# Kernel tuning notes

Hardware: AMD Instinct MI355X
Metric: run time of the kernel (lower is better)

Reference implementation:

```python
import jax, jax.numpy as jnp
import numpy as np


def setup_inputs() -> dict:
    key = jax.random.key(0)
    ks = jax.random.split(key, 7)
    b, t, c = 2, 2048, 1024
    s = 0.02  # keep pre-softmax logits in a sane range
    return {
        "query": jax.random.normal(ks[0], (b, t, c), jnp.float32),
        "key": jax.random.normal(ks[1], (b, t, c), jnp.float32),
        "value": jax.random.normal(ks[2], (b, t, c), jnp.float32),
        "in_proj_w": jax.random.normal(ks[3], (3 * c, c), jnp.float32) * s,
        "in_proj_b": jax.random.normal(ks[4], (3 * c,), jnp.float32) * s,
        "out_proj_w": jax.random.normal(ks[5], (c, c), jnp.float32) * s,
        "out_proj_b": jax.random.normal(ks[6], (c,), jnp.float32) * s,
        "window_size": 128,
    }


def reference(query, key, value, in_proj_w, in_proj_b, out_proj_w, out_proj_b, window_size):
    num_heads = 16
    b, t, c = query.shape
    hd = c // num_heads
    wq, wk, wv = in_proj_w[:c], in_proj_w[c:2 * c], in_proj_w[2 * c:]
    bq, bk, bv = in_proj_b[:c], in_proj_b[c:2 * c], in_proj_b[2 * c:]
    # project and split heads: [b, h, t, hd]
    q = (query @ wq.T + bq).reshape(b, t, num_heads, hd).transpose(0, 2, 1, 3)
    k = (key @ wk.T + bk).reshape(b, t, num_heads, hd).transpose(0, 2, 1, 3)
    v = (value @ wv.T + bv).reshape(b, t, num_heads, hd).transpose(0, 2, 1, 3)
    # NOTE: torch adds a *float* attn_mask to the logits. The original mask is
    # 1.0 inside the sliding window, 0.0 outside -- an additive +1 bias, NOT -inf.
    idx = jnp.arange(t)
    band = (jnp.abs(idx[:, None] - idx[None, :]) <= window_size).astype(q.dtype)  # [t, t]
    scale = 1.0 / jnp.sqrt(jnp.asarray(hd, q.dtype))
    logits = jnp.einsum("bhqd,bhkd->bhqk", q * scale, k) + band  # [b,h,t,t]
    attn = jax.nn.softmax(logits, axis=-1)
    out = jnp.einsum("bhqk,bhkd->bhqd", attn, v)  # [b,h,t,hd]
    out = out.transpose(0, 2, 1, 3).reshape(b, t, c)
    return out @ out_proj_w.T + out_proj_b
```

## Files before the change

kernel.cpp:

```cpp
#include <hip/hip_runtime.h>

typedef __attribute__((ext_vector_type(8)))  short short8;
typedef __attribute__((ext_vector_type(4)))  float f32x4;
typedef __attribute__((ext_vector_type(16))) float f32x16;
typedef __attribute__((ext_vector_type(2)))  unsigned uint2v;

constexpr int B  = 2;
constexpr int T  = 2048;
constexpr int C  = 1024;
constexpr int H  = 16;
constexpr int HD = 64;

__device__ inline unsigned bf16rne(float a){
  unsigned u = __builtin_bit_cast(unsigned, a);
  u += 0x7fffu + ((u >> 16) & 1u);
  return u >> 16;
}
__device__ inline unsigned bf16pair(float a, float b){
  unsigned ua = __builtin_bit_cast(unsigned, a); ua += 0x7fffu + ((ua >> 16) & 1u);
  unsigned ub = __builtin_bit_cast(unsigned, b); ub += 0x7fffu + ((ub >> 16) & 1u);
  return (ua >> 16) | (ub & 0xffff0000u);
}
__device__ inline void gll16(const void* g, void* l){
  __builtin_amdgcn_global_load_lds(
      (const __attribute__((address_space(1))) unsigned*)g,
      (__attribute__((address_space(3))) unsigned*)l, 16, 0, 0);
}
__device__ inline float exp2f_(float x){
#if __has_builtin(__builtin_amdgcn_exp2f)
  return __builtin_amdgcn_exp2f(x);
#else
  return __builtin_exp2f(x);
#endif
}

__global__ void convert_k(const float* __restrict__ ipw, const float* __restrict__ opw,
                          const float* __restrict__ q, const float* __restrict__ k,
                          const float* __restrict__ v, unsigned* __restrict__ dst)
{
  const int i = blockIdx.x * 256 + threadIdx.x;
  const long e = (long)i * 8;
  const float* src; long off;
  if      (e <  3145728) { src = ipw; off = e; }
  else if (e <  4194304) { src = opw; off = e - 3145728; }
  else if (e <  8388608) { src = q;   off = e - 4194304; }
  else if (e < 12582912) { src = k;   off = e - 8388608; }
  else                   { src = v;   off = e - 12582912; }
  const float4 x0 = *(const float4*)(src + off);
  const float4 x1 = *(const float4*)(src + off + 4);
  uint4 st;
  st.x = bf16pair(x0.x, x0.y); st.y = bf16pair(x0.z, x0.w);
  st.z = bf16pair(x1.x, x1.y); st.w = bf16pair(x1.z, x1.w);
  *(uint4*)(dst + (size_t)i*4) = st;
}

__global__ __launch_bounds__(256, 3) void gemm_qkv(
    const unsigned short* __restrict__ A0, const unsigned short* __restrict__ A1,
    const unsigned short* __restrict__ A2,
    const unsigned short* __restrict__ Wb, const float* __restrict__ bias,
    unsigned short* __restrict__ Qb, unsigned short* __restrict__ Kf,
    unsigned short* __restrict__ Vf)
{
  __shared__ __align__(16) char gsm[32768];
  unsigned short* As = (unsigned short*)gsm;
  unsigned short* Bs = (unsigned short*)(gsm + 16384);

  const int tid  = threadIdx.x, lane = tid & 63, wv = tid >> 6;
  const int wm   = wv & 1, wn = wv >> 1;
  const int bm   = blockIdx.x, bn = blockIdx.y;
  const int m16  = lane & 15, quad = lane >> 4;

  const int which = bn >> 3;
  const unsigned short* A = (which == 0) ? A0 : (which == 1 ? A1 : A2);

  f32x4 acc[4][4];
#pragma unroll
  for (int i = 0; i < 4; i++)
#pragma unroll
    for (int j = 0; j < 4; j++) acc[i][j] = (f32x4){0.f, 0.f, 0.f, 0.f};

  const int srow = wv * 32 + (lane >> 3);
  const int skp  = (((lane & 7) ^ (lane >> 3))) * 8;
  const int xr   = m16 & 7;

  for (int k0 = 0; k0 < 1024; k0 += 64) {
    __syncthreads();
#pragma unroll
    for (int p = 0; p < 4; p++) {
      gll16(A  + (size_t)(bm*128 + srow + p*8)*1024 + k0 + skp, (char*)As + wv*4096 + p*1024);
      gll16(Wb + (size_t)(bn*128 + srow + p*8)*1024 + k0 + skp, (char*)Bs + wv*4096 + p*1024);
    }
    __syncthreads();

#pragma unroll
    for (int kk = 0; kk < 2; kk++) {
      const int ch = ((kk*4 + quad) ^ xr) * 16;
      short8 af[4], bf[4];
#pragma unroll
      for (int i = 0; i < 4; i++)
        af[i] = *(const short8*)((const char*)As + (wm*64 + i*16 + m16)*128 + ch);
#pragma unroll
      for (int j = 0; j < 4; j++)
        bf[j] = *(const short8*)((const char*)Bs + (wn*64 + j*16 + m16)*128 + ch);
#pragma unroll
      for (int i = 0; i < 4; i++)
#pragma unroll
        for (int j = 0; j < 4; j++)
          acc[i][j] = __builtin_amdgcn_mfma_f32_16x16x32_bf16(af[i], bf[j], acc[i][j], 0,0,0);
    }
  }

  __syncthreads();
  float* Ls = (float*)gsm;
  const int hbase = (bn & 7) * 2;
  const int b = bm >> 4;
  const int tbase = (bm & 15) * 128;
  const float ksc = (which == 1) ? 0.18033688f : 1.0f;

  if (which < 2) {
#pragma unroll
    for (int j = 0; j < 4; ++j) {
      const float bj = bias[bn*128 + wn*64 + j*16 + m16] * ksc;
#pragma unroll
      for (int i = 0; i < 4; ++i) {
        const int m0 = wm*64 + i*16 + quad*4;
#pragma unroll
        for (int r = 0; r < 4; ++r)
          Ls[(m0 + r)*36 + wn*16 + m16] = __builtin_fmaf(acc[i][j][r], ksc, bj);
      }
      __syncthreads();
#pragma unroll
      for (int r2 = 0; r2 < 2; ++r2) {
        const int v = r2*256 + tid;
        const int m = v & 127, seg = v >> 7;
        const int wn2 = seg >> 1;
        const float* src = &Ls[m*36 + wn2*16 + (seg & 1)*8];
        const float4 f0 = *(const float4*)src;
        const float4 f1 = *(const float4*)(src + 4);
        uint4 st;
        st.x = bf16pair(f0.x, f0.y); st.y = bf16pair(f0.z, f0.w);
        st.z = bf16pair(f1.x, f1.y); st.w = bf16pair(f1.z, f1.w);
        const int bhh = b*16 + hbase + wn2;
        if (which == 0) {
          const int d0 = j*16 + (seg & 1)*8;
          *(uint4*)&Qb[((size_t)(bhh*2048) + tbase + m)*64 + d0] = st;
        } else {
          const int kt = (tbase + m) >> 6;
          const int wkk = (m >> 5) & 1, ln2 = m & 31;
          const int h2 = seg & 1;
          uint4* dp = (uint4*)Kf + ((size_t)(bhh*32 + kt)*8 + j*2 + wkk)*64 + h2*32 + ln2;
          *dp = st;
        }
      }
      __syncthreads();
    }
  } else {
#pragma unroll
    for (int j = 0; j < 4; ++j) {
      const float bj = bias[bn*128 + wn*64 + j*16 + m16];
      const int col = wn*16 + m16;
#pragma unroll
      for (int i = 0; i < 4; ++i) {
        f32x4 tv = acc[i][j];
        tv[0] += bj; tv[1] += bj; tv[2] += bj; tv[3] += bj;
        *(f32x4*)&Ls[col*132 + wm*64 + i*16 + quad*4] = tv;
      }
      __syncthreads();
#pragma unroll
      for (int r2 = 0; r2 < 2; ++r2) {
        const int v = r2*256 + tid;
        const int n = v >> 4, mseg = v & 15;
        const float* src = &Ls[n*132 + mseg*8];
        const float4 f0 = *(const float4*)src;
        const float4 f1 = *(const float4*)(src + 4);
        uint4 st;
        st.x = bf16pair(f0.x, f0.y); st.y = bf16pair(f0.z, f0.w);
        st.z = bf16pair(f1.x, f1.y); st.w = bf16pair(f1.z, f1.w);
        const int d = j*16 + (n & 15);
        const int bhh = b*16 + hbase + (n >> 4);
        const int t0 = tbase + mseg*8;
        const int kt = t0 >> 6, tc = (t0 & 63) >> 3;
        const int wkk = tc >> 2, cc = (tc >> 1) & 1, h2 = tc & 1;
        const int dt = d >> 5, ln2 = d & 31;
        uint4* dp = (uint4*)Vf + (size_t)(bhh*32 + kt)*512 + dt*256 + cc*128 + wkk*64 + h2*32 + ln2;
        *dp = st;
      }
      __syncthreads();
    }
  }
}

__global__ __launch_bounds__(256, 4) void gemm_out(
    const unsigned short* __restrict__ Ab, const unsigned short* __restrict__ Wb,
    const float* __restrict__ bias, float* __restrict__ outF)
{
  __shared__ __align__(16) char gsm[16384];
  unsigned short* As = (unsigned short*)gsm;
  unsigned short* Ws = (unsigned short*)(gsm + 8192);

  const int tid  = threadIdx.x, lane = tid & 63, wv = tid >> 6;
  const int bm   = blockIdx.x, bn = blockIdx.y;
  const int m16  = lane & 15, quad = lane >> 4;

  f32x4 acc[4];
#pragma unroll
  for (int i = 0; i < 4; i++) acc[i] = (f32x4){0.f, 0.f, 0.f, 0.f};

  const int srow = wv * 16 + (lane >> 3);
  const int skp  = (((lane & 7) ^ (lane >> 3))) * 8;
  const int xr   = m16 & 7;

  for (int k0 = 0; k0 < 1024; k0 += 64) {
    __syncthreads();
#pragma unroll
    for (int p = 0; p < 2; p++) {
      gll16(Ab + (size_t)(bm*64 + srow + p*8)*1024 + k0 + skp, (char*)As + wv*2048 + p*1024);
      gll16(Wb + (size_t)(bn*64 + srow + p*8)*1024 + k0 + skp, (char*)Ws + wv*2048 + p*1024);
    }
    __syncthreads();

#pragma unroll
    for (int kk = 0; kk < 2; kk++) {
      const int ch = ((kk*4 + quad) ^ xr) * 16;
      short8 af[4], bf;
#pragma unroll
      for (int i = 0; i < 4; i++)
        af[i] = *(const short8*)((const char*)As + (i*16 + m16)*128 + ch);
      bf = *(const short8*)((const char*)Ws + (wv*16 + m16)*128 + ch);
#pragma unroll
      for (int i = 0; i < 4; i++)
        acc[i] = __builtin_amdgcn_mfma_f32_16x16x32_bf16(af[i], bf, acc[i], 0,0,0);
    }
  }

  const int n_e = bn*64 + wv*16 + m16;
  const float bj = bias[n_e];
#pragma unroll
  for (int i = 0; i < 4; i++) {
    const int mbase = bm*64 + i*16 + quad*4;
#pragma unroll
    for (int r = 0; r < 4; r++)
      outF[(size_t)(mbase + r) * 1024 + n_e] = acc[i][r] + bj;
  }
}

__global__ __launch_bounds__(256, 3) void attn_k(
    const unsigned short* __restrict__ Qb, const unsigned short* __restrict__ Kf,
    const unsigned short* __restrict__ Vf, const int* __restrict__ wptr,
    unsigned short* __restrict__ ctx)
{
  __shared__ __align__(16) char smem[16896];
  float* Om   = (float*)smem;
  float* lbuf = (float*)(smem + 16384);

  const int tid = threadIdx.x, lane = tid & 63, wv = tid >> 6;
  const int wq = wv >> 1, wk = wv & 1;
  const int h = lane >> 5, ln = lane & 31;
  const int bh = blockIdx.x, qt = blockIdx.y;
  const int win = *wptr;
  const int q0 = qt * 64 + wq * 32;
  const size_t hb = (size_t)bh * T * HD;

  constexpr float LOG2E = 1.44269504f;

  short8 qf[4];
#pragma unroll
  for (int s = 0; s < 4; s++)
    qf[s] = *(const short8*)(Qb + hb + (size_t)(q0 + ln)*64 + s*16 + h*8);

  short8 onesv;
#pragma unroll
  for (int jj = 0; jj < 8; jj++) onesv[jj] = (short)0x3F80;

  f32x16 O0, O1, Lacc, Zv;
#pragma unroll
  for (int r = 0; r < 16; r++) { O0[r] = 0.f; O1[r] = 0.f; Lacc[r] = 0.f; Zv[r] = 0.f; }
  const int tq = q0 + ln;

  const uint4* kbase = (const uint4*)Kf + (size_t)bh*32*512 + wk*64 + lane;
  const uint4* vbase = (const uint4*)Vf + (size_t)bh*32*512 + wk*64 + lane;

  uint4 kA[4], vA[4];
#pragma unroll
  for (int s = 0; s < 4; s++) kA[s] = kbase[s*128];
#pragma unroll
  for (int u = 0; u < 4; u++) vA[u] = vbase[(u >> 1)*256 + (u & 1)*128];

  for (int kt = 0; kt < 32; ++kt) {
    f32x16 st;
#pragma unroll
    for (int s = 0; s < 4; s++) {
      const short8 kf2 = __builtin_bit_cast(short8, kA[s]);
      st = __builtin_amdgcn_mfma_f32_32x32x16_bf16(kf2, qf[s], (s == 0 ? Zv : st), 0, 0, 0);
    }
    if (kt < 31) {
      const size_t o = (size_t)(kt + 1) * 512;
#pragma unroll
      for (int s = 0; s < 4; s++) kA[s] = kbase[o + s*128];
    }

    const int kb = kt*64 + wk*32;
    int sep = 0;
    if (kb > q0 + 31) sep = kb - (q0 + 31);
    else if (q0 > kb + 31) sep = q0 - (kb + 31);
    const int d1 = kb + 31 - q0, d2 = q0 + 31 - kb;
    const int dmax = max(d1 < 0 ? -d1 : d1, d2 < 0 ? -d2 : d2);

    float pr[16];
    if (sep > win) {
#pragma unroll
      for (int r = 0; r < 16; r++) pr[r] = exp2f_(st[r]);
    } else if (dmax <= win) {
#pragma unroll
      for (int r = 0; r < 16; r++) pr[r] = exp2f_(st[r] + LOG2E);
    } else {
      const int tkb = kb + 4*h;
#pragma unroll
      for (int r = 0; r < 16; r++) {
        const int tk = tkb + (r & 3) + 8*(r >> 2);
        int dd = tq - tk; dd = dd < 0 ? -dd : dd;
        pr[r] = exp2f_(st[r] + (dd <= win ? LOG2E : 0.0f));
      }
    }

    unsigned pk[8];
#pragma unroll
    for (int g = 0; g < 8; g++)
      pk[g] = __builtin_amdgcn_perm(__builtin_bit_cast(unsigned, pr[2*g+1]),
                                    __builtin_bit_cast(unsigned, pr[2*g]),
                                    0x07060302u);

#pragma unroll
    for (int c = 0; c < 2; c++) {
      const uint2v s02 = __builtin_amdgcn_permlane32_swap(pk[4*c+0], pk[4*c+2], false, false);
      const uint2v s13 = __builtin_amdgcn_permlane32_swap(pk[4*c+1], pk[4*c+3], false, false);
      union { unsigned u[4]; short8 v; } P;
      P.u[0] = s02[0];
      P.u[1] = s13[0];
      P.u[2] = s02[1];
      P.u[3] = s13[1];
#pragma unroll
      for (int dt = 0; dt < 2; dt++) {
        const short8 vf2 = __builtin_bit_cast(short8, vA[dt*2 + c]);
        if (dt == 0) O0 = __builtin_amdgcn_mfma_f32_32x32x16_bf16(P.v, vf2, O0, 0,0,0);
        else         O1 = __builtin_amdgcn_mfma_f32_32x32x16_bf16(P.v, vf2, O1, 0,0,0);
      }
      Lacc = __builtin_amdgcn_mfma_f32_32x32x16_bf16(P.v, onesv, Lacc, 0,0,0);
    }

    if (kt < 31) {
      const size_t o = (size_t)(kt + 1) * 512;
#pragma unroll
      for (int u = 0; u < 4; u++) vA[u] = vbase[o + (u >> 1)*256 + (u & 1)*128];
    }
  }

  __syncthreads();
  if (wk == 1) {
#pragma unroll
    for (int r = 0; r < 16; r++) {
      Om[wq*2048 + r*64 + lane]        = O0[r];
      Om[wq*2048 + (16 + r)*64 + lane] = O1[r];
    }
    if (ln == 0) {
#pragma unroll
      for (int r = 0; r < 16; r++)
        lbuf[wq*32 + (r & 3) + 8*(r >> 2) + 4*h] = Lacc[r];
    }
  }
  __syncthreads();
  if (wk == 0) {
    const int b = bh >> 4, hh = bh & 15;
#pragma unroll
    for (int r = 0; r < 16; r++) {
      const int qrow = (r & 3) + 8*(r >> 2) + 4*h;
      const float lt = Lacc[r] + lbuf[wq*32 + qrow];
      const float linv = 1.0f / lt;
      const int t = q0 + qrow;
      const float o0 = (O0[r] + Om[wq*2048 + r*64 + lane]) * linv;
      const float o1 = (O1[r] + Om[wq*2048 + (16 + r)*64 + lane]) * linv;
      unsigned short* cp = ctx + (size_t)(b*2048 + t)*1024 + hh*64;
      cp[ln]      = (unsigned short)bf16rne(o0);
      cp[32 + ln] = (unsigned short)bf16rne(o1);
    }
  }
}

extern "C" void kernel_launch(void* const* d_in, const int* in_sizes, int n_in,
                              void* d_out, int out_size, void* d_ws, size_t ws_size,
                              hipStream_t stream)
{
  const float* query = (const float*)d_in[0];
  const float* key   = (const float*)d_in[1];
  const float* value = (const float*)d_in[2];
  const float* ipw   = (const float*)d_in[3];
  const float* ipb   = (const float*)d_in[4];
  const float* opw   = (const float*)d_in[5];
  const float* opb   = (const float*)d_in[6];
  const int*   win   = (const int*)d_in[7];

  char* ws = (char*)d_ws;
  unsigned short* Winbf  = (unsigned short*)(ws);
  unsigned short* Woutbf = (unsigned short*)(ws + 6291456);
  unsigned short* Qin    = (unsigned short*)(ws + 8388608);
  unsigned short* Kin    = (unsigned short*)(ws + 16777216);
  unsigned short* Vin    = (unsigned short*)(ws + 25165824);
  unsigned short* Qb     = (unsigned short*)(ws + 33554432);
  unsigned short* Kf     = (unsigned short*)(ws + 41943040);
  unsigned short* Vf     = (unsigned short*)(ws + 50331648);
  unsigned short* ctx    = (unsigned short*)(ws + 58720256);

  convert_k<<<8192, 256, 0, stream>>>(ipw, opw, query, key, value, (unsigned*)ws);

  gemm_qkv<<<dim3(32, 24), 256, 0, stream>>>(
      Qin, Kin, Vin, Winbf, ipb, Qb, Kf, Vf);

  attn_k<<<dim3(32, 32), 256, 0, stream>>>(Qb, Kf, Vf, win, ctx);

  gemm_out<<<dim3(64, 16), 256, 0, stream>>>(
      ctx, Woutbf, opb, (float*)d_out);
}
```

Baseline: 213.2 us.

## Fuse fp32-to-bf16 activation conversion into QKV GEMM A-tile loads

The separate conversion kernel now handles only the weights. The QKV GEMM reads fp32 activations straight from global memory into registers, converts them to bf16, and writes them to LDS, prefetching the next k-tile in registers. This removes a full pass over the activations (an fp32 read plus a bf16 write and re-read) and one launch's worth of work. The cost is more register pressure, and the A operand is now twice as wide to read per GEMM tile. Since each A tile is reread by 24 column blocks, fp32 global traffic for A rises.

```diff
diff --git a/kernel.cpp b/kernel.cpp
--- a/kernel.cpp
+++ b/kernel.cpp
@@ -34,18 +34,14 @@
 #endif
 }
 
-__global__ void convert_k(const float* __restrict__ ipw, const float* __restrict__ opw,
-                          const float* __restrict__ q, const float* __restrict__ k,
-                          const float* __restrict__ v, unsigned* __restrict__ dst)
+__global__ void convert_w(const float* __restrict__ ipw, const float* __restrict__ opw,
+                          unsigned* __restrict__ dst)
 {
   const int i = blockIdx.x * 256 + threadIdx.x;
   const long e = (long)i * 8;
   const float* src; long off;
-  if      (e <  3145728) { src = ipw; off = e; }
-  else if (e <  4194304) { src = opw; off = e - 3145728; }
-  else if (e <  8388608) { src = q;   off = e - 4194304; }
-  else if (e < 12582912) { src = k;   off = e - 8388608; }
-  else                   { src = v;   off = e - 12582912; }
+  if (e < 3145728) { src = ipw; off = e; }
+  else             { src = opw; off = e - 3145728; }
   const float4 x0 = *(const float4*)(src + off);
   const float4 x1 = *(const float4*)(src + off + 4);
   uint4 st;
@@ -55,8 +51,8 @@
 }
 
 __global__ __launch_bounds__(256, 3) void gemm_qkv(
-    const unsigned short* __restrict__ A0, const unsigned short* __restrict__ A1,
-    const unsigned short* __restrict__ A2,
+    const float* __restrict__ A0, const float* __restrict__ A1,
+    const float* __restrict__ A2,
     const unsigned short* __restrict__ Wb, const float* __restrict__ bias,
     unsigned short* __restrict__ Qb, unsigned short* __restrict__ Kf,
     unsigned short* __restrict__ Vf)
@@ -71,7 +67,7 @@
   const int m16  = lane & 15, quad = lane >> 4;
 
   const int which = bn >> 3;
-  const unsigned short* A = (which == 0) ? A0 : (which == 1 ? A1 : A2);
+  const float* A = (which == 0) ? A0 : (which == 1 ? A1 : A2);
 
   f32x4 acc[4][4];
 #pragma unroll
@@ -83,12 +79,35 @@
   const int skp  = (((lane & 7) ^ (lane >> 3))) * 8;
   const int xr   = m16 & 7;
 
+  const float* ap[4];
+#pragma unroll
+  for (int p = 0; p < 4; p++)
+    ap[p] = A + (size_t)(bm*128 + srow + p*8)*1024 + skp;
+
+  float4 ar0[4], ar1[4];
+#pragma unroll
+  for (int p = 0; p < 4; p++) {
+    ar0[p] = *(const float4*)(ap[p]);
+    ar1[p] = *(const float4*)(ap[p] + 4);
+  }
+
   for (int k0 = 0; k0 < 1024; k0 += 64) {
     __syncthreads();
 #pragma unroll
+    for (int p = 0; p < 4; p++)
+      gll16(Wb + (size_t)(bn*128 + srow + p*8)*1024 + k0 + skp, (char*)Bs + wv*4096 + p*1024);
+#pragma unroll
     for (int p = 0; p < 4; p++) {
-      gll16(A  + (size_t)(bm*128 + srow + p*8)*1024 + k0 + skp, (char*)As + wv*4096 + p*1024);
-      gll16(Wb + (size_t)(bn*128 + srow + p*8)*1024 + k0 + skp, (char*)Bs + wv*4096 + p*1024);
+      uint4 st;
+      st.x = bf16pair(ar0[p].x, ar0[p].y); st.y = bf16pair(ar0[p].z, ar0[p].w);
+      st.z = bf16pair(ar1[p].x, ar1[p].y); st.w = bf16pair(ar1[p].z, ar1[p].w);
+      *(uint4*)((char*)As + wv*4096 + p*1024 + lane*16) = st;
+    }
+    const int k0n = (k0 + 64 < 1024) ? k0 + 64 : 0;
+#pragma unroll
+    for (int p = 0; p < 4; p++) {
+      ar0[p] = *(const float4*)(ap[p] + k0n);
+      ar1[p] = *(const float4*)(ap[p] + k0n + 4);
     }
     __syncthreads();
 
@@ -402,18 +421,15 @@
   char* ws = (char*)d_ws;
   unsigned short* Winbf  = (unsigned short*)(ws);
   unsigned short* Woutbf = (unsigned short*)(ws + 6291456);
-  unsigned short* Qin    = (unsigned short*)(ws + 8388608);
-  unsigned short* Kin    = (unsigned short*)(ws + 16777216);
-  unsigned short* Vin    = (unsigned short*)(ws + 25165824);
   unsigned short* Qb     = (unsigned short*)(ws + 33554432);
   unsigned short* Kf     = (unsigned short*)(ws + 41943040);
   unsigned short* Vf     = (unsigned short*)(ws + 50331648);
   unsigned short* ctx    = (unsigned short*)(ws + 58720256);
 
-  convert_k<<<8192, 256, 0, stream>>>(ipw, opw, query, key, value, (unsigned*)ws);
+  convert_w<<<2048, 256, 0, stream>>>(ipw, opw, (unsigned*)ws);
 
   gemm_qkv<<<dim3(32, 24), 256, 0, stream>>>(
-      Qin, Kin, Vin, Winbf, ipb, Qb, Kf, Vf);
+      query, key, value, Winbf, ipb, Qb, Kf, Vf);
 
   attn_k<<<dim3(32, 32), 256, 0, stream>>>(Qb, Kf, Vf, win, ctx);
 
```

New measurement: 206.9 us. 3.0% less time.

## Double-buffer LDS tiles in QKV and output GEMMs with prefetch two ahead

Applied to the files above, without the earlier changes.

Both projection GEMMs now use two LDS buffers and issue global-to-LDS loads for tile kt+2 while computing tile kt. Partial vmcnt waits and raw s_barriers replace the two full __syncthreads per iteration. The goal is to hide global load latency behind the MFMA work. The cost is doubled LDS per block, and the QKV launch bound drops from 3 to 2 blocks per CU, which lowers occupancy.

```diff
diff --git a/kernel.cpp b/kernel.cpp
--- a/kernel.cpp
+++ b/kernel.cpp
@@ -54,17 +54,14 @@
   *(uint4*)(dst + (size_t)i*4) = st;
 }
 
-__global__ __launch_bounds__(256, 3) void gemm_qkv(
+__global__ __launch_bounds__(256, 2) void gemm_qkv(
     const unsigned short* __restrict__ A0, const unsigned short* __restrict__ A1,
     const unsigned short* __restrict__ A2,
     const unsigned short* __restrict__ Wb, const float* __restrict__ bias,
     unsigned short* __restrict__ Qb, unsigned short* __restrict__ Kf,
     unsigned short* __restrict__ Vf)
 {
-  __shared__ __align__(16) char gsm[32768];
-  unsigned short* As = (unsigned short*)gsm;
-  unsigned short* Bs = (unsigned short*)(gsm + 16384);
-
+  __shared__ __align__(16) char gsm[65536];
   const int tid  = threadIdx.x, lane = tid & 63, wv = tid >> 6;
   const int wm   = wv & 1, wn = wv >> 1;
   const int bm   = blockIdx.x, bn = blockIdx.y;
@@ -83,31 +80,50 @@
   const int skp  = (((lane & 7) ^ (lane >> 3))) * 8;
   const int xr   = m16 & 7;
 
-  for (int k0 = 0; k0 < 1024; k0 += 64) {
-    __syncthreads();
+  auto stage = [&](int kt, int b){
+    const int k0 = kt * 64;
 #pragma unroll
     for (int p = 0; p < 4; p++) {
-      gll16(A  + (size_t)(bm*128 + srow + p*8)*1024 + k0 + skp, (char*)As + wv*4096 + p*1024);
-      gll16(Wb + (size_t)(bn*128 + srow + p*8)*1024 + k0 + skp, (char*)Bs + wv*4096 + p*1024);
-    }
-    __syncthreads();
-
+      gll16(A  + (size_t)(bm*128 + srow + p*8)*1024 + k0 + skp,
+            (char*)gsm + b*16384 + wv*4096 + p*1024);
+      gll16(Wb + (size_t)(bn*128 + srow + p*8)*1024 + k0 + skp,
+            (char*)gsm + 32768 + b*16384 + wv*4096 + p*1024);
+    }
+  };
+
+  stage(0, 0);
+  stage(1, 1);
+
+  for (int kt = 0; kt < 16; ++kt) {
+    const int cur = kt & 1;
+    if (kt < 15) asm volatile("s_waitcnt vmcnt(8)" ::: "memory");
+    else         asm volatile("s_waitcnt vmcnt(0)" ::: "memory");
+    __builtin_amdgcn_sched_barrier(0);
+    __builtin_amdgcn_s_barrier();
+    __builtin_amdgcn_sched_barrier(0);
+
+    const char* Asb = (const char*)gsm + cur*16384;
+    const char* Bsb = (const char*)gsm + 32768 + cur*16384;
 #pragma unroll
     for (int kk = 0; kk < 2; kk++) {
       const int ch = ((kk*4 + quad) ^ xr) * 16;
       short8 af[4], bf[4];
 #pragma unroll
       for (int i = 0; i < 4; i++)
-        af[i] = *(const short8*)((const char*)As + (wm*64 + i*16 + m16)*128 + ch);
+        af[i] = *(const short8*)(Asb + (wm*64 + i*16 + m16)*128 + ch);
 #pragma unroll
       for (int j = 0; j < 4; j++)
-        bf[j] = *(const short8*)((const char*)Bs + (wn*64 + j*16 + m16)*128 + ch);
+        bf[j] = *(const short8*)(Bsb + (wn*64 + j*16 + m16)*128 + ch);
 #pragma unroll
       for (int i = 0; i < 4; i++)
 #pragma unroll
         for (int j = 0; j < 4; j++)
           acc[i][j] = __builtin_amdgcn_mfma_f32_16x16x32_bf16(af[i], bf[j], acc[i][j], 0,0,0);
     }
+    __builtin_amdgcn_sched_barrier(0);
+    __builtin_amdgcn_s_barrier();
+    __builtin_amdgcn_sched_barrier(0);
+    if (kt + 2 < 16) stage(kt + 2, cur);
   }
 
   __syncthreads();
@@ -194,10 +210,7 @@
     const unsigned short* __restrict__ Ab, const unsigned short* __restrict__ Wb,
     const float* __restrict__ bias, float* __restrict__ outF)
 {
-  __shared__ __align__(16) char gsm[16384];
-  unsigned short* As = (unsigned short*)gsm;
-  unsigned short* Ws = (unsigned short*)(gsm + 8192);
-
+  __shared__ __align__(16) char gsm[32768];
   const int tid  = threadIdx.x, lane = tid & 63, wv = tid >> 6;
   const int bm   = blockIdx.x, bn = blockIdx.y;
   const int m16  = lane & 15, quad = lane >> 4;
@@ -210,27 +223,46 @@
   const int skp  = (((lane & 7) ^ (lane >> 3))) * 8;
   const int xr   = m16 & 7;
 
-  for (int k0 = 0; k0 < 1024; k0 += 64) {
-    __syncthreads();
+  auto stage = [&](int kt, int b){
+    const int k0 = kt * 64;
 #pragma unroll
     for (int p = 0; p < 2; p++) {
-      gll16(Ab + (size_t)(bm*64 + srow + p*8)*1024 + k0 + skp, (char*)As + wv*2048 + p*1024);
-      gll16(Wb + (size_t)(bn*64 + srow + p*8)*1024 + k0 + skp, (char*)Ws + wv*2048 + p*1024);
-    }
-    __syncthreads();
-
+      gll16(Ab + (size_t)(bm*64 + srow + p*8)*1024 + k0 + skp,
+            (char*)gsm + b*8192 + wv*2048 + p*1024);
+      gll16(Wb + (size_t)(bn*64 + srow + p*8)*1024 + k0 + skp,
+            (char*)gsm + 16384 + b*8192 + wv*2048 + p*1024);
+    }
+  };
+
+  stage(0, 0);
+  stage(1, 1);
+
+  for (int kt = 0; kt < 16; ++kt) {
+    const int cur = kt & 1;
+    if (kt < 15) asm volatile("s_waitcnt vmcnt(4)" ::: "memory");
+    else         asm volatile("s_waitcnt vmcnt(0)" ::: "memory");
+    __builtin_amdgcn_sched_barrier(0);
+    __builtin_amdgcn_s_barrier();
+    __builtin_amdgcn_sched_barrier(0);
+
+    const char* Asb = (const char*)gsm + cur*8192;
+    const char* Wsb = (const char*)gsm + 16384 + cur*8192;
 #pragma unroll
     for (int kk = 0; kk < 2; kk++) {
       const int ch = ((kk*4 + quad) ^ xr) * 16;
       short8 af[4], bf;
 #pragma unroll
       for (int i = 0; i < 4; i++)
-        af[i] = *(const short8*)((const char*)As + (i*16 + m16)*128 + ch);
-      bf = *(const short8*)((const char*)Ws + (wv*16 + m16)*128 + ch);
+        af[i] = *(const short8*)(Asb + (i*16 + m16)*128 + ch);
+      bf = *(const short8*)(Wsb + (wv*16 + m16)*128 + ch);
 #pragma unroll
       for (int i = 0; i < 4; i++)
         acc[i] = __builtin_amdgcn_mfma_f32_16x16x32_bf16(af[i], bf, acc[i], 0,0,0);
     }
+    __builtin_amdgcn_sched_barrier(0);
+    __builtin_amdgcn_s_barrier();
+    __builtin_amdgcn_sched_barrier(0);
+    if (kt + 2 < 16) stage(kt + 2, cur);
   }
 
   const int n_e = bn*64 + wv*16 + m16;
```

New measurement: 205.2 us. 1.04x faster.
